# Kernel tuning notes

Measured on AMD Instinct MI355X. Metric: run time of the kernel, lower is better.

## Reference

```python
import jax, jax.numpy as jnp
import numpy as np

B, S, D = 4, 2048, 1024

def setup_inputs() -> dict:
    key = jax.random.key(0)
    kx, kq, kk, kv = jax.random.split(key, 4)
    scale = 0.02
    return {
        'x': jax.random.normal(kx, (B, S, D), dtype=jnp.float32),
        'wq': jax.random.normal(kq, (D, D), dtype=jnp.float32) * scale,
        'wk': jax.random.normal(kk, (D, D), dtype=jnp.float32) * scale,
        'wv': jax.random.normal(kv, (D, D), dtype=jnp.float32) * scale,
    }

def reference(x, wq, wk, wv):
    # QKV projections (no bias): nn.Linear applies x @ W^T; here wq is already [d_in, d_out]
    q = jnp.einsum('bsd,de->bse', x, wq)
    k = jnp.einsum('bsd,de->bse', x, wk)
    v = jnp.einsum('bsd,de->bse', x, wv)
    d_k = k.shape[-1]
    scores = jnp.einsum('bqd,bkd->bqk', q, k) / jnp.sqrt(jnp.float32(d_k))
    s = x.shape[1]
    causal = jnp.tril(jnp.ones((s, s), dtype=bool))  # True = keep
    scores = jnp.where(causal[None, :, :], scores, -jnp.inf)
    attn = jax.nn.softmax(scores, axis=-1)
    # dropout p=0.0 -> identity
    return jnp.einsum('bqk,bkd->bqd', attn, v)
```

## Files before the change

kernel.cpp:

```cpp
#include <hip/hip_runtime.h>
#include <hip/hip_bf16.h>


typedef __attribute__((ext_vector_type(8))) short bf16x8;
typedef __attribute__((ext_vector_type(4))) float f32x4;

#define GLOAD_LDS16(g, l)                                                     \
    __builtin_amdgcn_global_load_lds(                                         \
        (const __attribute__((address_space(1))) void*)(g),                   \
        (__attribute__((address_space(3))) void*)(l), 16, 0, 0)

__device__ __forceinline__ short f2bf(float f) {
    union { float f; unsigned u; } v; v.f = f;
    unsigned r = v.u + 0x7FFFu + ((v.u >> 16) & 1u);
    return (short)(r >> 16);
}

__global__ __launch_bounds__(256) void convx(const float* __restrict__ x,
                                             short* __restrict__ xb, int n4) {
    int i = blockIdx.x * 256 + threadIdx.x;
    if (i < n4) {
        float4 v = ((const float4*)x)[i];
        short4 o;
        o.x = f2bf(v.x); o.y = f2bf(v.y); o.z = f2bf(v.z); o.w = f2bf(v.w);
        ((short4*)xb)[i] = o;
    }
}

__global__ __launch_bounds__(256) void wtrans(const float* __restrict__ wq,
                                              const float* __restrict__ wk,
                                              const float* __restrict__ wv,
                                              short* __restrict__ wt) {
    int w = blockIdx.z;
    const float* W = (w == 0) ? wq : (w == 1) ? wk : wv;
    short* O = wt + (size_t)w * 1048576;
    int n0 = blockIdx.x * 64, k0 = blockIdx.y * 64;
    __shared__ float tile[64][65];
    int t = threadIdx.x;
#pragma unroll
    for (int i = 0; i < 16; ++i) {
        int idx = t + i * 256;
        int r = idx >> 6, c = idx & 63;
        tile[r][c] = W[(size_t)(k0 + r) * 1024 + n0 + c];
    }
    __syncthreads();
#pragma unroll
    for (int i = 0; i < 16; ++i) {
        int idx = t + i * 256;
        int r = idx >> 6, c = idx & 63;
        O[(size_t)(n0 + r) * 1024 + k0 + c] = f2bf(tile[c][r]);
    }
}

template <int MODE>
__global__ __launch_bounds__(256, 2) void gemm128(
    const short* __restrict__ A0, int lda0, long long sA,
    const short* __restrict__ B0, int ldb0, long long sB,
    void* __restrict__ C0, float scale,
    const short* __restrict__ Av, const short* __restrict__ Bv,
    short* __restrict__ Cv) {

    int bid;
    {
        const int nblk = gridDim.x;
        const int raw = blockIdx.x;
        bid = (raw & 7) * (nblk >> 3) + (raw >> 3);
    }

    int m0, n0, z = 0, lda = lda0, ldb = ldb0;
    const short* Ab;
    const short* Bb;
    bool isVT = false;

    if (MODE == 0) {
        m0 = (bid >> 4) * 128;
        n0 = (bid & 15) * 128;
        Ab = A0; Bb = B0;
    } else if (MODE == 1) {
        if (bid < 544) {
            z = bid >> 7;
            z = bid / 136;
            int f = bid - z * 136;
            int mt = (int)((sqrtf(8.f * f + 1.f) - 1.f) * 0.5f);
            if (mt * (mt + 1) / 2 > f) --mt;
            if ((mt + 1) * (mt + 2) / 2 <= f) ++mt;
            int nt_ = f - mt * (mt + 1) / 2;
            m0 = mt * 128; n0 = nt_ * 128;
            Ab = A0 + (size_t)z * sA;
            Bb = B0 + (size_t)z * sB;
        } else {
            isVT = true;
            int v = bid - 544;
            m0 = (v >> 6) * 128;
            n0 = (v & 63) * 128;
            Ab = Av; Bb = Bv; lda = 1024; ldb = 1024;
        }
    } else {
        z = bid >> 7;
        int rem = bid & 127;
        m0 = (rem >> 3) * 128;
        n0 = (rem & 7) * 128;
        Ab = A0 + (size_t)z * sA;
        Bb = B0 + (size_t)z * sB;
    }

    const int tid = threadIdx.x;
    const int lane = tid & 63;
    const int wid = tid >> 6;
    const int wm = wid >> 1, wn = wid & 1;

    __shared__ __align__(16) short As[2][8192];
    __shared__ __align__(16) short Bs[2][8192];

    f32x4 acc[4][4] = {};

    const int Kend = (MODE == 2) ? (m0 + 128) : 1024;
    const int nt = Kend >> 6;

    const int srow = tid >> 3;
    const int sl = (tid & 7) ^ (srow & 7);
    const short* Agp = Ab + (size_t)(m0 + srow) * lda + sl * 8;
    const short* Bgp = Bb + (size_t)(n0 + srow) * ldb + sl * 8;

#define SA(kt, bf)                                                            \
    do {                                                                      \
        const int _k = (kt) << 6;                                             \
        GLOAD_LDS16(Agp + _k,                     &As[bf][tid * 8]);          \
        GLOAD_LDS16(Agp + _k + (size_t)32 * lda,  &As[bf][2048 + tid * 8]);   \
        GLOAD_LDS16(Agp + _k + (size_t)64 * lda,  &As[bf][4096 + tid * 8]);   \
        GLOAD_LDS16(Agp + _k + (size_t)96 * lda,  &As[bf][6144 + tid * 8]);   \
    } while (0)
#define SB(kt, bf)                                                            \
    do {                                                                      \
        const int _k = (kt) << 6;                                             \
        GLOAD_LDS16(Bgp + _k,                     &Bs[bf][tid * 8]);          \
        GLOAD_LDS16(Bgp + _k + (size_t)32 * ldb,  &Bs[bf][2048 + tid * 8]);   \
        GLOAD_LDS16(Bgp + _k + (size_t)64 * ldb,  &Bs[bf][4096 + tid * 8]);   \
        GLOAD_LDS16(Bgp + _k + (size_t)96 * ldb,  &Bs[bf][6144 + tid * 8]);   \
    } while (0)

    const int r = lane & 15;
    const int g = lane >> 4;

#define LDA4(dst, bf, kk)                                                     \
    _Pragma("unroll") for (int q = 0; q < 4; ++q) {                           \
        const int rr = wm * 64 + q * 16 + r;                                  \
        dst[q] = *(const bf16x8*)&As[bf][rr * 64 +                            \
                                         ((((kk)*4 + g) ^ (rr & 7))) * 8];    \
    }
#define LDB4(dst, bf, kk)                                                     \
    _Pragma("unroll") for (int q = 0; q < 4; ++q) {                           \
        const int rb = wn * 64 + q * 16 + r;                                  \
        dst[q] = *(const bf16x8*)&Bs[bf][rb * 64 +                            \
                                         ((((kk)*4 + g) ^ (rb & 7))) * 8];    \
    }
#define LGKM0()                                                               \
    asm volatile("s_waitcnt lgkmcnt(0)" ::: "memory");                        \
    __builtin_amdgcn_sched_barrier(0)
#define VM0() asm volatile("s_waitcnt vmcnt(0)" ::: "memory")
#define BAR() __builtin_amdgcn_s_barrier()
#define MF(ar, br)                                                            \
    _Pragma("unroll") for (int mi = 0; mi < 4; ++mi)                          \
        _Pragma("unroll") for (int ni = 0; ni < 4; ++ni)                      \
            acc[mi][ni] = __builtin_amdgcn_mfma_f32_16x16x32_bf16(            \
                ar[mi], br[ni], acc[mi][ni], 0, 0, 0);

    SA(0, 0); SB(0, 0);
    VM0();
    BAR();

    int buf = 0;
    for (int t = 0; t < nt - 1; ++t) {
        const int nb = buf ^ 1;
        SA(t + 1, nb); SB(t + 1, nb);
        bf16x8 a[4], b[4];
        LDA4(a, buf, 0); LDB4(b, buf, 0);
        LGKM0();
        MF(a, b);
        LDA4(a, buf, 1); LDB4(b, buf, 1);
        LGKM0();
        MF(a, b);
        VM0();
        BAR();
        buf = nb;
    }
    {
        bf16x8 a[4], b[4];
        LDA4(a, buf, 0); LDB4(b, buf, 0);
        LGKM0();
        MF(a, b);
        LDA4(a, buf, 1); LDB4(b, buf, 1);
        LGKM0();
        MF(a, b);
    }

    const int r4 = (lane >> 4) * 4;
#pragma unroll
    for (int mi = 0; mi < 4; ++mi) {
#pragma unroll
        for (int ni = 0; ni < 4; ++ni) {
            int col = n0 + wn * 64 + ni * 16 + r;
#pragma unroll
            for (int i = 0; i < 4; ++i) {
                int rr = m0 + wm * 64 + mi * 16 + r4 + i;
                float v = acc[mi][ni][i];
                if (MODE == 0) {
                    ((short*)C0)[(size_t)(col >> 10) * 8388608 +
                                 (size_t)rr * 1024 + (col & 1023)] = f2bf(v);
                } else if (MODE == 1) {
                    if (isVT) {
                        Cv[(size_t)(col >> 11) * 2097152 +
                           (size_t)rr * 2048 + (col & 2047)] = f2bf(v);
                    } else if (col <= rr) {
                        ((float*)C0)[(size_t)z * 4194304 +
                                     (size_t)rr * 2048 + col] = v * scale;
                    }
                } else {
                    ((float*)C0)[(size_t)z * 2097152 +
                                 (size_t)rr * 1024 + col] = v;
                }
            }
        }
    }
#undef SA
#undef SB
#undef LDA4
#undef LDB4
#undef LGKM0
#undef VM0
#undef BAR
#undef MF
}

__global__ __launch_bounds__(256) void softmax_causal(float* __restrict__ scores) {
    int row = blockIdx.x;
    int b = row >> 11, i = row & 2047;
    float* srow = scores + ((size_t)b * 2048 + i) * 2048;
    short* arow = (short*)srow;
    __shared__ float sv[2048];
    __shared__ float red[8];
    int t = threadIdx.x;
    int L = i + 1;

    float mx = -1e30f;
    for (int j = t; j < L; j += 256) {
        float v = srow[j];
        sv[j] = v;
        mx = fmaxf(mx, v);
    }
#pragma unroll
    for (int o = 32; o > 0; o >>= 1) mx = fmaxf(mx, __shfl_down(mx, o));
    if ((t & 63) == 0) red[t >> 6] = mx;
    __syncthreads();
    mx = fmaxf(fmaxf(red[0], red[1]), fmaxf(red[2], red[3]));

    float sum = 0.f;
    for (int j = t; j < L; j += 256) {
        float e = __expf(sv[j] - mx);
        sv[j] = e;
        sum += e;
    }
#pragma unroll
    for (int o = 32; o > 0; o >>= 1) sum += __shfl_down(sum, o);
    if ((t & 63) == 0) red[4 + (t >> 6)] = sum;
    __syncthreads();
    sum = red[4] + red[5] + red[6] + red[7];
    float rinv = 1.0f / sum;

    int Lpad = (i | 255) + 1;
    for (int j = t; j < Lpad; j += 256) {
        float p = (j < L) ? sv[j] * rinv : 0.0f;
        arow[j] = f2bf(p);
    }
}

extern "C" void kernel_launch(void* const* d_in, const int* in_sizes, int n_in,
                              void* d_out, int out_size, void* d_ws, size_t ws_size,
                              hipStream_t stream) {
    const float* x  = (const float*)d_in[0];
    const float* wq = (const float*)d_in[1];
    const float* wk = (const float*)d_in[2];
    const float* wv = (const float*)d_in[3];
    float* out = (float*)d_out;

    short* ws16 = (short*)d_ws;
    short* xb = ws16;
    short* wt = xb + 8388608;
    short* qb = wt + 3145728;
    short* kb = qb + 8388608;
    short* vt = kb + 8388608;
    float* scores = (float*)(vt + 8388608);

    convx<<<8192, 256, 0, stream>>>(x, xb, 2097152);
    wtrans<<<dim3(16, 16, 3), 256, 0, stream>>>(wq, wk, wv, wt);
    gemm128<0><<<1024, 256, 0, stream>>>(
        xb, 1024, 0LL, wt, 1024, 0LL, qb, 1.0f, nullptr, nullptr, nullptr);
    gemm128<1><<<1056, 256, 0, stream>>>(
        qb, 1024, 2097152LL, kb, 1024, 2097152LL, scores, 0.03125f,
        wt + 2097152, xb, vt);
    softmax_causal<<<8192, 256, 0, stream>>>(scores);
    gemm128<2><<<512, 256, 0, stream>>>(
        (const short*)scores, 4096, 8388608LL, vt, 2048, 2097152LL, out, 1.0f,
        nullptr, nullptr, nullptr);
}
```

Measured before the change: 172.4 us.

## Fold Wq·Wkᵀ into one matrix, vectorize softmax, reorder PV tile schedule

Instead of projecting both Q and K, the code precomputes M = Wq·Wkᵀ scaled by 1/sqrt(d) in a small 1024×1024 GEMM. It then computes T = X·M, so the scores become T·Xᵀ. This cuts the projection work from two big GEMMs to one plus a small one and skips writing K. Softmax now uses float4 loads and stores with padding to 128 instead of 256. The PV GEMM assigns causal tiles from heavy to light to balance load. Folding the weights changes the bf16 rounding path, so accuracy can differ slightly.

```diff
diff --git a/kernel.cpp b/kernel.cpp
--- a/kernel.cpp
+++ b/kernel.cpp
@@ -27,13 +27,8 @@
     }
 }
 
-__global__ __launch_bounds__(256) void wtrans(const float* __restrict__ wq,
-                                              const float* __restrict__ wk,
-                                              const float* __restrict__ wv,
-                                              short* __restrict__ wt) {
-    int w = blockIdx.z;
-    const float* W = (w == 0) ? wq : (w == 1) ? wk : wv;
-    short* O = wt + (size_t)w * 1048576;
+__global__ __launch_bounds__(256) void wtrans(const float* __restrict__ W,
+                                              short* __restrict__ O) {
     int n0 = blockIdx.x * 64, k0 = blockIdx.y * 64;
     __shared__ float tile[64][65];
     int t = threadIdx.x;
@@ -60,48 +55,47 @@
     const short* __restrict__ Av, const short* __restrict__ Bv,
     short* __restrict__ Cv) {
 
-    int bid;
-    {
-        const int nblk = gridDim.x;
-        const int raw = blockIdx.x;
-        bid = (raw & 7) * (nblk >> 3) + (raw >> 3);
-    }
-
     int m0, n0, z = 0, lda = lda0, ldb = ldb0;
     const short* Ab;
     const short* Bb;
     bool isVT = false;
 
-    if (MODE == 0) {
-        m0 = (bid >> 4) * 128;
-        n0 = (bid & 15) * 128;
-        Ab = A0; Bb = B0;
-    } else if (MODE == 1) {
-        if (bid < 544) {
-            z = bid >> 7;
-            z = bid / 136;
-            int f = bid - z * 136;
-            int mt = (int)((sqrtf(8.f * f + 1.f) - 1.f) * 0.5f);
-            if (mt * (mt + 1) / 2 > f) --mt;
-            if ((mt + 1) * (mt + 2) / 2 <= f) ++mt;
-            int nt_ = f - mt * (mt + 1) / 2;
-            m0 = mt * 128; n0 = nt_ * 128;
-            Ab = A0 + (size_t)z * sA;
-            Bb = B0 + (size_t)z * sB;
-        } else {
-            isVT = true;
-            int v = bid - 544;
-            m0 = (v >> 6) * 128;
-            n0 = (v & 63) * 128;
-            Ab = Av; Bb = Bv; lda = 1024; ldb = 1024;
-        }
-    } else {
-        z = bid >> 7;
-        int rem = bid & 127;
-        m0 = (rem >> 3) * 128;
-        n0 = (rem & 7) * 128;
+    if (MODE == 2) {
+        int i = blockIdx.x;
+        int j = i & 255;
+        int mt = (i < 256) ? (15 - (j >> 5)) : (j >> 5);
+        z = (j >> 3) & 3;
+        m0 = mt * 128;
+        n0 = (j & 7) * 128;
         Ab = A0 + (size_t)z * sA;
         Bb = B0 + (size_t)z * sB;
+    } else {
+        const int nblk = gridDim.x;
+        const int raw = blockIdx.x;
+        int bid = (raw & 7) * (nblk >> 3) + (raw >> 3);
+        if (MODE == 5) {
+            m0 = (bid >> 3) * 128;
+            n0 = (bid & 7) * 128;
+            Ab = A0; Bb = B0;
+        } else {
+            if (bid < 544) {
+                z = bid / 136;
+                int f = bid - z * 136;
+                int mt = (int)((sqrtf(8.f * f + 1.f) - 1.f) * 0.5f);
+                if (mt * (mt + 1) / 2 > f) --mt;
+                if ((mt + 1) * (mt + 2) / 2 <= f) ++mt;
+                int nt_ = f - mt * (mt + 1) / 2;
+                m0 = mt * 128; n0 = nt_ * 128;
+                Ab = A0 + (size_t)z * sA;
+                Bb = B0 + (size_t)z * sB;
+            } else {
+                isVT = true;
+                int v = bid - 544;
+                m0 = (v >> 6) * 128;
+                n0 = (v & 63) * 128;
+                Ab = Av; Bb = Bv; lda = 1024; ldb = 1024;
+            }
+        }
     }
 
     const int tid = threadIdx.x;
@@ -204,16 +198,15 @@
             for (int i = 0; i < 4; ++i) {
                 int rr = m0 + wm * 64 + mi * 16 + r4 + i;
                 float v = acc[mi][ni][i];
-                if (MODE == 0) {
-                    ((short*)C0)[(size_t)(col >> 10) * 8388608 +
-                                 (size_t)rr * 1024 + (col & 1023)] = f2bf(v);
+                if (MODE == 5) {
+                    ((short*)C0)[(size_t)rr * 1024 + col] = f2bf(v * scale);
                 } else if (MODE == 1) {
                     if (isVT) {
                         Cv[(size_t)(col >> 11) * 2097152 +
                            (size_t)rr * 2048 + (col & 2047)] = f2bf(v);
                     } else if (col <= rr) {
                         ((float*)C0)[(size_t)z * 4194304 +
-                                     (size_t)rr * 2048 + col] = v * scale;
+                                     (size_t)rr * 2048 + col] = v;
                     }
                 } else {
                     ((float*)C0)[(size_t)z * 2097152 +
@@ -237,16 +230,22 @@
     int b = row >> 11, i = row & 2047;
     float* srow = scores + ((size_t)b * 2048 + i) * 2048;
     short* arow = (short*)srow;
-    __shared__ float sv[2048];
+    __shared__ float4 sv4[512];
     __shared__ float red[8];
     int t = threadIdx.x;
     int L = i + 1;
+    int nv = (L + 3) >> 2;
 
     float mx = -1e30f;
-    for (int j = t; j < L; j += 256) {
-        float v = srow[j];
-        sv[j] = v;
-        mx = fmaxf(mx, v);
+    for (int v = t; v < nv; v += 256) {
+        float4 w = ((const float4*)srow)[v];
+        int base = v << 2;
+        w.x = (base + 0 < L) ? w.x : -1e30f;
+        w.y = (base + 1 < L) ? w.y : -1e30f;
+        w.z = (base + 2 < L) ? w.z : -1e30f;
+        w.w = (base + 3 < L) ? w.w : -1e30f;
+        sv4[v] = w;
+        mx = fmaxf(mx, fmaxf(fmaxf(w.x, w.y), fmaxf(w.z, w.w)));
     }
 #pragma unroll
     for (int o = 32; o > 0; o >>= 1) mx = fmaxf(mx, __shfl_down(mx, o));
@@ -255,10 +254,15 @@
     mx = fmaxf(fmaxf(red[0], red[1]), fmaxf(red[2], red[3]));
 
     float sum = 0.f;
-    for (int j = t; j < L; j += 256) {
-        float e = __expf(sv[j] - mx);
-        sv[j] = e;
-        sum += e;
+    for (int v = t; v < nv; v += 256) {
+        float4 w = sv4[v];
+        float4 e;
+        e.x = __expf(w.x - mx);
+        e.y = __expf(w.y - mx);
+        e.z = __expf(w.z - mx);
+        e.w = __expf(w.w - mx);
+        sv4[v] = e;
+        sum += (e.x + e.y) + (e.z + e.w);
     }
 #pragma unroll
     for (int o = 32; o > 0; o >>= 1) sum += __shfl_down(sum, o);
@@ -267,10 +271,15 @@
     sum = red[4] + red[5] + red[6] + red[7];
     float rinv = 1.0f / sum;
 
-    int Lpad = (i | 255) + 1;
-    for (int j = t; j < Lpad; j += 256) {
-        float p = (j < L) ? sv[j] * rinv : 0.0f;
-        arow[j] = f2bf(p);
+    int npad = ((i | 127) + 1) >> 2;
+    for (int v = t; v < npad; v += 256) {
+        float4 w = (v < nv) ? sv4[v] : float4{0.f, 0.f, 0.f, 0.f};
+        short4 o4;
+        o4.x = f2bf(w.x * rinv);
+        o4.y = f2bf(w.y * rinv);
+        o4.z = f2bf(w.z * rinv);
+        o4.w = f2bf(w.w * rinv);
+        ((short4*)arow)[v] = o4;
     }
 }
 
@@ -284,20 +293,28 @@
     float* out = (float*)d_out;
 
     short* ws16 = (short*)d_ws;
-    short* xb = ws16;
-    short* wt = xb + 8388608;
-    short* qb = wt + 3145728;
-    short* kb = qb + 8388608;
-    short* vt = kb + 8388608;
+    short* xb  = ws16;
+    short* wqb = xb + 8388608;
+    short* wkb = wqb + 1048576;
+    short* wtv = wkb + 1048576;
+    short* Mt  = wtv + 1048576;
+    short* tb  = Mt + 1048576;
+    short* vt  = tb + 8388608;
     float* scores = (float*)(vt + 8388608);
 
     convx<<<8192, 256, 0, stream>>>(x, xb, 2097152);
-    wtrans<<<dim3(16, 16, 3), 256, 0, stream>>>(wq, wk, wv, wt);
-    gemm128<0><<<1024, 256, 0, stream>>>(
-        xb, 1024, 0LL, wt, 1024, 0LL, qb, 1.0f, nullptr, nullptr, nullptr);
+    convx<<<1024, 256, 0, stream>>>(wq, wqb, 262144);
+    convx<<<1024, 256, 0, stream>>>(wk, wkb, 262144);
+    wtrans<<<dim3(16, 16, 1), 256, 0, stream>>>(wv, wtv);
+    gemm128<5><<<64, 256, 0, stream>>>(
+        wkb, 1024, 0LL, wqb, 1024, 0LL, Mt, 0.03125f,
+        nullptr, nullptr, nullptr);
+    gemm128<5><<<512, 256, 0, stream>>>(
+        xb, 1024, 0LL, Mt, 1024, 0LL, tb, 1.0f,
+        nullptr, nullptr, nullptr);
     gemm128<1><<<1056, 256, 0, stream>>>(
-        qb, 1024, 2097152LL, kb, 1024, 2097152LL, scores, 0.03125f,
-        wt + 2097152, xb, vt);
+        tb, 1024, 2097152LL, xb, 1024, 2097152LL, scores, 1.0f,
+        wtv, xb, vt);
     softmax_causal<<<8192, 256, 0, stream>>>(scores);
     gemm128<2><<<512, 256, 0, stream>>>(
         (const short*)scores, 4096, 8388608LL, vt, 2048, 2097152LL, out, 1.0f,
```

Result: no change. 171.4 us (-0.6%).
